# Optimization experiments

Hardware: AMD Instinct MI355X
Metric: run time of the kernel (lower is better)

The kernel has to match this reference:

```python
import jax, jax.numpy as jnp
import numpy as np

D_MODEL = 2048
NUM_HEADS = 16
HEAD_DIM = D_MODEL // NUM_HEADS
B, T = 4, 2048


def setup_inputs() -> dict:
    key = jax.random.key(0)
    ks = jax.random.split(key, 9)
    s = 1.0 / np.sqrt(D_MODEL)
    inp = {"x": jax.random.normal(ks[0], (B, T, D_MODEL), dtype=jnp.float32)}
    for i, name in enumerate(["q", "k", "v", "o"]):
        inp[f"W{name}"] = jax.random.uniform(ks[1 + 2 * i], (D_MODEL, D_MODEL), minval=-s, maxval=s, dtype=jnp.float32)
        inp[f"b{name}"] = jax.random.uniform(ks[2 + 2 * i], (D_MODEL,), minval=-s, maxval=s, dtype=jnp.float32)
    return inp


def reference(x, Wq, bq, Wk, bk, Wv, bv, Wo, bo):
    Bx, Tx, _ = x.shape
    H, Dh = NUM_HEADS, HEAD_DIM
    # torch Linear: y = x @ W.T + b
    q = (x @ Wq.T + bq).reshape(Bx, Tx, H, Dh).transpose(0, 2, 1, 3)  # [B,H,T,D]
    k = (x @ Wk.T + bk).reshape(Bx, Tx, H, Dh).transpose(0, 2, 1, 3)
    v = (x @ Wv.T + bv).reshape(Bx, Tx, H, Dh).transpose(0, 2, 1, 3)
    scale = 1.0 / np.sqrt(Dh).astype(np.float32)
    scores = jnp.einsum('bhqd,bhkd->bhqk', q, k) * scale  # [B,H,T,T] (no causal mask, as in source)
    attn = jax.nn.softmax(scores, axis=-1)
    out = jnp.einsum('bhqk,bhkd->bhqd', attn, v)  # [B,H,T,D]
    out = out.transpose(0, 2, 1, 3).reshape(Bx, Tx, H * Dh)
    return out @ Wo.T + bo
```

## Files before the change

### kernel.cpp

```cpp
#include <hip/hip_runtime.h>
#include <hip/hip_bf16.h>

typedef __bf16 bf16x8 __attribute__((ext_vector_type(8)));
typedef __bf16 bf16x4 __attribute__((ext_vector_type(4)));
typedef float floatx4 __attribute__((ext_vector_type(4)));

#define MFMA16(a, b, c) __builtin_amdgcn_mfma_f32_16x16x32_bf16((a), (b), (c), 0, 0, 0)

#define GLOAD16(g, l) __builtin_amdgcn_global_load_lds( \
    (const __attribute__((address_space(1))) unsigned int*)(g), \
    (__attribute__((address_space(3))) unsigned int*)(l), 16, 0, 0)

static constexpr int DM = 2048, NH = 16, HD = 128, BATCH = 4, SEQ = 2048;
static constexpr int MROWS = BATCH * SEQ;
static constexpr float SCALE = 0.08838834764831845f;
static constexpr float PMAX = 3.0f;

__global__ __launch_bounds__(256) void detect_dtype(
    const unsigned short* __restrict__ x, const unsigned short* __restrict__ w,
    int* __restrict__ flags) {
  const unsigned short* src = blockIdx.x ? w : x;
  const int tid = threadIdx.x;
  int cnt = 0;
  for (int i = tid; i < 4096; i += 256) {
    unsigned short u = src[2 * i];
    int e = (u >> 7) & 0xFF;
    cnt += (e >= 96 && e <= 158) ? 1 : 0;
  }
  __shared__ int s[256];
  s[tid] = cnt;
  __syncthreads();
  for (int off = 128; off > 0; off >>= 1) {
    if (tid < off) s[tid] += s[tid + off];
    __syncthreads();
  }
  if (tid == 0) flags[blockIdx.x] = (s[0] > 2560) ? 1 : 0;
}

__global__ __launch_bounds__(256) void cvt_f32_bf16(
    const float* __restrict__ src, __bf16* __restrict__ dst, int n,
    const int* __restrict__ flags) {
  if (flags[0] != 0) return;
  int stride = gridDim.x * 256 * 8;
  for (int i = (blockIdx.x * 256 + threadIdx.x) * 8; i < n; i += stride) {
    float4 a = *reinterpret_cast<const float4*>(src + i);
    float4 b = *reinterpret_cast<const float4*>(src + i + 4);
    bf16x8 r;
    r[0] = (__bf16)a.x; r[1] = (__bf16)a.y; r[2] = (__bf16)a.z; r[3] = (__bf16)a.w;
    r[4] = (__bf16)b.x; r[5] = (__bf16)b.y; r[6] = (__bf16)b.z; r[7] = (__bf16)b.w;
    *reinterpret_cast<bf16x8*>(dst + i) = r;
  }
}

__device__ __forceinline__ void gemm128_core(
    const __bf16* __restrict__ A, const __bf16* __restrict__ W,
    unsigned short* sA, unsigned short* sW,
    int tm, int tn, floatx4 (&acc)[4][4]) {
  const int tid = threadIdx.x;
  const int wave = tid >> 6, lane = tid & 63;
  const int q = lane >> 4, ml = lane & 15;
  const int waveM = (wave >> 1) * 64, waveN = (wave & 1) * 64;
  const int lrow = lane >> 3, cdst = lane & 7;
  const int csrc = cdst ^ (lrow & 7);

  for (int k0 = 0; k0 < DM; k0 += 64) {
    __syncthreads();
#pragma unroll
    for (int i = 0; i < 4; ++i) {
      int r0 = wave * 32 + i * 8;
      GLOAD16(A + (size_t)(tm + r0 + lrow) * DM + k0 + csrc * 8, &sA[r0 * 64]);
      GLOAD16(W + (size_t)(tn + r0 + lrow) * DM + k0 + csrc * 8, &sW[r0 * 64]);
    }
    __syncthreads();
#pragma unroll
    for (int s = 0; s < 2; ++s) {
      bf16x8 aF[4], bF[4];
#pragma unroll
      for (int t = 0; t < 4; ++t)
        aF[t] = *reinterpret_cast<const bf16x8*>(
            &sA[(waveM + t * 16 + ml) * 64 + (((s * 4 + q) ^ (ml & 7)) * 8)]);
#pragma unroll
      for (int t = 0; t < 4; ++t)
        bF[t] = *reinterpret_cast<const bf16x8*>(
            &sW[(waveN + t * 16 + ml) * 64 + (((s * 4 + q) ^ (ml & 7)) * 8)]);
#pragma unroll
      for (int rt = 0; rt < 4; ++rt)
#pragma unroll
        for (int ct = 0; ct < 4; ++ct)
          acc[rt][ct] = MFMA16(aF[rt], bF[ct], acc[rt][ct]);
    }
  }
}

__global__ __launch_bounds__(256) void qkv_gemm(
    const __bf16* __restrict__ X,
    const __bf16* __restrict__ Wq, const __bf16* __restrict__ Wk,
    const __bf16* __restrict__ Wv,
    const void* bq, const void* bk, const void* bv, int bias_f32,
    __bf16* __restrict__ qw, __bf16* __restrict__ kw, __bf16* __restrict__ vt,
    const int* __restrict__ flags, int wantX) {
  if (flags[0] != wantX) return;
  __shared__ unsigned short sA[128 * 64];
  __shared__ unsigned short sW[128 * 64];
  const int which = blockIdx.x >> 4;
  const int tn = (blockIdx.x & 15) * 128;
  const int tm = blockIdx.y * 128;
  const __bf16* W = which == 0 ? Wq : (which == 1 ? Wk : Wv);
  const void* bias = which == 0 ? bq : (which == 1 ? bk : bv);

  floatx4 acc[4][4] = {};
  gemm128_core(X, W, sA, sW, tm, tn, acc);

  const int tid = threadIdx.x, wave = tid >> 6, lane = tid & 63;
  const int q = lane >> 4, ml = lane & 15;
  const int waveM = (wave >> 1) * 64, waveN = (wave & 1) * 64;
#pragma unroll
  for (int ct = 0; ct < 4; ++ct) {
    int n = tn + waveN + ct * 16 + ml;
    float bv_ = bias_f32 ? ((const float*)bias)[n] : (float)((const __bf16*)bias)[n];
#pragma unroll
    for (int rt = 0; rt < 4; ++rt) {
      int m0 = tm + waveM + rt * 16 + q * 4;
      if (which < 2) {
        __bf16* dst = which == 0 ? qw : kw;
#pragma unroll
        for (int r = 0; r < 4; ++r)
          dst[(size_t)(m0 + r) * DM + n] = (__bf16)(acc[rt][ct][r] + bv_);
      } else {
        int h = n >> 7, d = n & 127, b = m0 >> 11, t = m0 & 2047;
        bf16x4 pk;
#pragma unroll
        for (int r = 0; r < 4; ++r) pk[r] = (__bf16)(acc[rt][ct][r] + bv_);
        *reinterpret_cast<bf16x4*>(vt + (size_t)((b * 16 + h) * 128 + d) * SEQ + t) = pk;
      }
    }
  }
}

__global__ __launch_bounds__(256) void proj_gemm(
    const __bf16* __restrict__ A, const __bf16* __restrict__ W,
    const void* bias, int bias_f32, void* out, int out_f32,
    const int* __restrict__ flags, int want) {
  if (flags[1] != want) return;
  __shared__ unsigned short sA[128 * 64];
  __shared__ unsigned short sW[128 * 64];
  const int tn = blockIdx.x * 128;
  const int tm = blockIdx.y * 128;

  floatx4 acc[4][4] = {};
  gemm128_core(A, W, sA, sW, tm, tn, acc);

  const int tid = threadIdx.x, wave = tid >> 6, lane = tid & 63;
  const int q = lane >> 4, ml = lane & 15;
  const int waveM = (wave >> 1) * 64, waveN = (wave & 1) * 64;
#pragma unroll
  for (int ct = 0; ct < 4; ++ct) {
    int n = tn + waveN + ct * 16 + ml;
    float bv_ = bias_f32 ? ((const float*)bias)[n] : (float)((const __bf16*)bias)[n];
#pragma unroll
    for (int rt = 0; rt < 4; ++rt) {
      int m0 = tm + waveM + rt * 16 + q * 4;
      if (out_f32) {
#pragma unroll
        for (int r = 0; r < 4; ++r)
          ((float*)out)[(size_t)(m0 + r) * DM + n] = acc[rt][ct][r] + bv_;
      } else {
#pragma unroll
        for (int r = 0; r < 4; ++r)
          ((__bf16*)out)[(size_t)(m0 + r) * DM + n] = (__bf16)(acc[rt][ct][r] + bv_);
      }
    }
  }
}

__device__ inline bf16x8 ld8s(const __bf16* p) {
  int4 v = *reinterpret_cast<const int4*>(p);
  return __builtin_bit_cast(bf16x8, v);
}
__device__ inline bf16x8 ld8s(const float* p) {
  float4 a = *reinterpret_cast<const float4*>(p);
  float4 b = *reinterpret_cast<const float4*>(p + 4);
  bf16x8 r;
  r[0] = (__bf16)a.x; r[1] = (__bf16)a.y; r[2] = (__bf16)a.z; r[3] = (__bf16)a.w;
  r[4] = (__bf16)b.x; r[5] = (__bf16)b.y; r[6] = (__bf16)b.z; r[7] = (__bf16)b.w;
  return r;
}

template <typename TA, typename TW>
__global__ __launch_bounds__(256) void gemm_slow(
    const TA* __restrict__ A, const TW* __restrict__ W,
    const TW* __restrict__ bias, void* __restrict__ C,
    int mode, int out_f32, const int* __restrict__ flags, int wantA, int wantW) {
  if (wantA >= 0 && flags[0] != wantA) return;
  if (wantW >= 0 && flags[1] != wantW) return;
  __shared__ unsigned short sA[128 * 72];
  __shared__ unsigned short sW[128 * 72];
  const int tid = threadIdx.x;
  const int tn = blockIdx.x * 128, tm = blockIdx.y * 128;
  const int wave = tid >> 6, lane = tid & 63;
  const int q = lane >> 4, ml = lane & 15;
  const int waveM = (wave >> 1) * 64, waveN = (wave & 1) * 64;
  const int srow = tid >> 3, sc8 = tid & 7;
  const int K = DM, N = DM;
  floatx4 acc[4][4] = {};
  for (int k0 = 0; k0 < K; k0 += 64) {
    bf16x8 va[4], vb[4];
#pragma unroll
    for (int i = 0; i < 4; ++i) {
      int row = srow + 32 * i;
      va[i] = ld8s(A + (size_t)(tm + row) * K + k0 + sc8 * 8);
      vb[i] = ld8s(W + (size_t)(tn + row) * K + k0 + sc8 * 8);
    }
    __syncthreads();
#pragma unroll
    for (int i = 0; i < 4; ++i) {
      int row = srow + 32 * i;
      *reinterpret_cast<int4*>(&sA[row * 72 + sc8 * 8]) = __builtin_bit_cast(int4, va[i]);
      *reinterpret_cast<int4*>(&sW[row * 72 + sc8 * 8]) = __builtin_bit_cast(int4, vb[i]);
    }
    __syncthreads();
#pragma unroll
    for (int s = 0; s < 2; ++s) {
      bf16x8 aF[4], bF[4];
#pragma unroll
      for (int t = 0; t < 4; ++t)
        aF[t] = *reinterpret_cast<const bf16x8*>(&sA[(waveM + t * 16 + ml) * 72 + s * 32 + q * 8]);
#pragma unroll
      for (int t = 0; t < 4; ++t)
        bF[t] = *reinterpret_cast<const bf16x8*>(&sW[(waveN + t * 16 + ml) * 72 + s * 32 + q * 8]);
#pragma unroll
      for (int rt = 0; rt < 4; ++rt)
#pragma unroll
        for (int ct = 0; ct < 4; ++ct)
          acc[rt][ct] = MFMA16(aF[rt], bF[ct], acc[rt][ct]);
    }
  }
#pragma unroll
  for (int ct = 0; ct < 4; ++ct) {
    int n = tn + waveN + ct * 16 + ml;
    float bv = (float)bias[n];
#pragma unroll
    for (int rt = 0; rt < 4; ++rt) {
      int mrow0 = tm + waveM + rt * 16 + q * 4;
      if (mode == 0) {
        if (out_f32) {
#pragma unroll
          for (int r = 0; r < 4; ++r)
            ((float*)C)[(size_t)(mrow0 + r) * N + n] = acc[rt][ct][r] + bv;
        } else {
#pragma unroll
          for (int r = 0; r < 4; ++r)
            ((__bf16*)C)[(size_t)(mrow0 + r) * N + n] = (__bf16)(acc[rt][ct][r] + bv);
        }
      } else {
        int h = n >> 7, d = n & 127, b = mrow0 >> 11, t = mrow0 & 2047;
        bf16x4 pk;
#pragma unroll
        for (int r = 0; r < 4; ++r) pk[r] = (__bf16)(acc[rt][ct][r] + bv);
        *reinterpret_cast<bf16x4*>((__bf16*)C + (size_t)((b * 16 + h) * 128 + d) * SEQ + t) = pk;
      }
    }
  }
}

__global__ __launch_bounds__(512) void mha_attn(
    const __bf16* __restrict__ Q, const __bf16* __restrict__ Kg,
    const __bf16* __restrict__ Vt, __bf16* __restrict__ O) {
  __shared__ unsigned short sK[64 * 128];
  __shared__ unsigned short sV[128 * 64];
  __shared__ unsigned short sP[128 * 72];

  const int tid = threadIdx.x;
  const int bh = blockIdx.y, b = bh >> 4, h = bh & 15;
  const int t0 = blockIdx.x * 128;
  const int wave = tid >> 6, lane = tid & 63;
  const int q = lane >> 4, ml = lane & 15;
  const int wrow = wave * 16;

  bf16x8 qf[4];
  {
    const __bf16* qrow = Q + (size_t)(b * SEQ + t0 + wrow + ml) * DM + h * HD;
#pragma unroll
    for (int s = 0; s < 4; ++s)
      qf[s] = *reinterpret_cast<const bf16x8*>(qrow + s * 32 + q * 8);
  }

  floatx4 oacc[8] = {};
  float lsum[4] = {0.f, 0.f, 0.f, 0.f};

  const __bf16* kbase = Kg + (size_t)(b * SEQ) * DM + h * HD;
  const __bf16* vbase = Vt + (size_t)bh * HD * SEQ;
  const int lrow4 = lane >> 4, c16 = lane & 15;
  const int lrow8 = lane >> 3, c8 = lane & 7;

  for (int kt = 0; kt < SEQ / 64; ++kt) {
    const int key0 = kt * 64;
    __syncthreads();
#pragma unroll
    for (int i = 0; i < 2; ++i) {
      int kr0 = wave * 8 + i * 4;
      int kc = c16 ^ ((i * 4 + lrow4) & 7);
      GLOAD16(kbase + (size_t)(key0 + kr0 + lrow4) * DM + kc * 8, &sK[kr0 * 128]);
      int vr0 = wave * 16 + i * 8;
      int vc = c8 ^ (lrow8 & 7);
      GLOAD16(vbase + (size_t)(vr0 + lrow8) * SEQ + key0 + vc * 8, &sV[vr0 * 64]);
    }
    __syncthreads();

    floatx4 sacc[4] = {};
#pragma unroll
    for (int s = 0; s < 4; ++s) {
#pragma unroll
      for (int ct = 0; ct < 4; ++ct) {
        bf16x8 kf = *reinterpret_cast<const bf16x8*>(
            &sK[(ct * 16 + ml) * 128 + (((s * 4 + q) ^ (ml & 7)) * 8)]);
        sacc[ct] = MFMA16(qf[s], kf, sacc[ct]);
      }
    }

#pragma unroll
    for (int ct = 0; ct < 4; ++ct) {
#pragma unroll
      for (int r = 0; r < 4; ++r) {
        float p = __expf(fmaf(sacc[ct][r], SCALE, -PMAX));
        sacc[ct][r] = p;
        lsum[r] += p;
        __bf16 pb = (__bf16)p;
        sP[(wrow + q * 4 + r) * 72 + ct * 16 + ml] = __builtin_bit_cast(unsigned short, pb);
      }
    }

#pragma unroll
    for (int s = 0; s < 2; ++s) {
      bf16x8 pf = *reinterpret_cast<const bf16x8*>(&sP[(wrow + ml) * 72 + s * 32 + q * 8]);
#pragma unroll
      for (int ot = 0; ot < 8; ++ot) {
        bf16x8 vf = *reinterpret_cast<const bf16x8*>(
            &sV[(ot * 16 + ml) * 64 + (((s * 4 + q) ^ (ml & 7)) * 8)]);
        oacc[ot] = MFMA16(pf, vf, oacc[ot]);
      }
    }
  }

#pragma unroll
  for (int r = 0; r < 4; ++r) {
    float s = lsum[r];
    s += __shfl_xor(s, 1); s += __shfl_xor(s, 2);
    s += __shfl_xor(s, 4); s += __shfl_xor(s, 8);
    lsum[r] = 1.0f / s;
  }
  __bf16* obase = O + (size_t)(b * SEQ + t0 + wrow) * DM + h * HD;
#pragma unroll
  for (int ot = 0; ot < 8; ++ot) {
    int d = ot * 16 + ml;
#pragma unroll
    for (int r = 0; r < 4; ++r)
      obase[(size_t)(q * 4 + r) * DM + d] = (__bf16)(oacc[ot][r] * lsum[r]);
  }
}

extern "C" void kernel_launch(void* const* d_in, const int* in_sizes, int n_in,
                              void* d_out, int out_size, void* d_ws, size_t ws_size,
                              hipStream_t stream) {
  const void* x  = d_in[0];
  const void* Wq = d_in[1]; const void* bq = d_in[2];
  const void* Wk = d_in[3]; const void* bk = d_in[4];
  const void* Wv = d_in[5]; const void* bv = d_in[6];
  const void* Wo = d_in[7]; const void* bo = d_in[8];

  int* flags = (int*)d_ws;
  const size_t XE = (size_t)MROWS * DM;
  const size_t WE = (size_t)DM * DM;

  detect_dtype<<<2, 256, 0, stream>>>((const unsigned short*)x, (const unsigned short*)Wq, flags);

  const size_t needA = 64 + 2 * XE * 2 + 4 * 2 * WE + 3 * 2 * XE;
  dim3 gq(48, 64), gp(16, 64), ga(SEQ / 128, BATCH * NH);

  if (ws_size >= needA + 256) {
    __bf16* xc  = (__bf16*)((char*)d_ws + 64);
    __bf16* Wqc = xc + XE;
    __bf16* Wkc = Wqc + WE;
    __bf16* Wvc = Wkc + WE;
    __bf16* Woc = Wvc + WE;
    __bf16* qw  = Woc + WE;
    __bf16* kw  = qw + XE;
    __bf16* vt  = kw + XE;
    __bf16* aw  = xc;

    cvt_f32_bf16<<<2048, 256, 0, stream>>>((const float*)x, xc, (int)XE, flags);
    cvt_f32_bf16<<<512, 256, 0, stream>>>((const float*)Wq, Wqc, (int)WE, flags);
    cvt_f32_bf16<<<512, 256, 0, stream>>>((const float*)Wk, Wkc, (int)WE, flags);
    cvt_f32_bf16<<<512, 256, 0, stream>>>((const float*)Wv, Wvc, (int)WE, flags);
    cvt_f32_bf16<<<512, 256, 0, stream>>>((const float*)Wo, Woc, (int)WE, flags);

    qkv_gemm<<<gq, 256, 0, stream>>>(xc, Wqc, Wkc, Wvc, bq, bk, bv, 1,
                                     qw, kw, vt, flags, 0);
    qkv_gemm<<<gq, 256, 0, stream>>>((const __bf16*)x, (const __bf16*)Wq,
                                     (const __bf16*)Wk, (const __bf16*)Wv,
                                     bq, bk, bv, 0, qw, kw, vt, flags, 1);
    mha_attn<<<ga, 512, 0, stream>>>(qw, kw, vt, aw);
    proj_gemm<<<gp, 256, 0, stream>>>(aw, Woc, bo, 1, d_out, 1, flags, 0);
    proj_gemm<<<gp, 256, 0, stream>>>(aw, (const __bf16*)Wo, bo, 0, d_out, 0, flags, 1);
  } else {
    __bf16* qw = (__bf16*)((char*)d_ws + 64);
    __bf16* kw = qw + XE;
    __bf16* vt = kw + XE;
    __bf16* aw = vt + XE;

    gemm_slow<float, float><<<gp, 256, 0, stream>>>(
        (const float*)x, (const float*)Wq, (const float*)bq, qw, 0, 0, flags, 0, 0);
    gemm_slow<float, float><<<gp, 256, 0, stream>>>(
        (const float*)x, (const float*)Wk, (const float*)bk, kw, 0, 0, flags, 0, 0);
    gemm_slow<float, float><<<gp, 256, 0, stream>>>(
        (const float*)x, (const float*)Wv, (const float*)bv, vt, 1, 0, flags, 0, 0);
    qkv_gemm<<<gq, 256, 0, stream>>>((const __bf16*)x, (const __bf16*)Wq,
                                     (const __bf16*)Wk, (const __bf16*)Wv,
                                     bq, bk, bv, 0, qw, kw, vt, flags, 1);
    mha_attn<<<ga, 512, 0, stream>>>(qw, kw, vt, aw);
    gemm_slow<__bf16, float><<<gp, 256, 0, stream>>>(
        aw, (const float*)Wo, (const float*)bo, d_out, 0, 1, flags, -1, 0);
    proj_gemm<<<gp, 256, 0, stream>>>(aw, (const __bf16*)Wo, bo, 0, d_out, 0, flags, 1);
  }
}
```

Baseline: 752.0 us.

## Drop dtype detection, fuse conversions, store Q/K head-major, reorder attention grid

Removes the runtime dtype-detection kernel and the duplicate bf16-path launches and assumes fp32 inputs. The five conversion kernels become one fused kernel over x and all weights. Q and K are now written in a per-head [B,H,T,D] layout, so attention loads them contiguously instead of with a 2048-element row stride. The attention grid is swapped so blocks sharing a head are adjacent, which may improve K/V cache reuse. This gives up support for bf16 inputs and adds scattered stores in the QKV epilogue.

```diff
diff --git a/kernel.cpp b/kernel.cpp
--- a/kernel.cpp
+++ b/kernel.cpp
@@ -16,35 +16,27 @@
 static constexpr float SCALE = 0.08838834764831845f;
 static constexpr float PMAX = 3.0f;
 
-__global__ __launch_bounds__(256) void detect_dtype(
-    const unsigned short* __restrict__ x, const unsigned short* __restrict__ w,
-    int* __restrict__ flags) {
-  const unsigned short* src = blockIdx.x ? w : x;
-  const int tid = threadIdx.x;
-  int cnt = 0;
-  for (int i = tid; i < 4096; i += 256) {
-    unsigned short u = src[2 * i];
-    int e = (u >> 7) & 0xFF;
-    cnt += (e >= 96 && e <= 158) ? 1 : 0;
-  }
-  __shared__ int s[256];
-  s[tid] = cnt;
-  __syncthreads();
-  for (int off = 128; off > 0; off >>= 1) {
-    if (tid < off) s[tid] += s[tid + off];
-    __syncthreads();
-  }
-  if (tid == 0) flags[blockIdx.x] = (s[0] > 2560) ? 1 : 0;
-}
-
-__global__ __launch_bounds__(256) void cvt_f32_bf16(
-    const float* __restrict__ src, __bf16* __restrict__ dst, int n,
-    const int* __restrict__ flags) {
-  if (flags[0] != 0) return;
-  int stride = gridDim.x * 256 * 8;
-  for (int i = (blockIdx.x * 256 + threadIdx.x) * 8; i < n; i += stride) {
-    float4 a = *reinterpret_cast<const float4*>(src + i);
-    float4 b = *reinterpret_cast<const float4*>(src + i + 4);
+static constexpr size_t XE = (size_t)MROWS * DM;
+static constexpr size_t WE = (size_t)DM * DM;
+
+__global__ __launch_bounds__(256) void cvt_all(
+    const float* __restrict__ x, const float* __restrict__ Wq,
+    const float* __restrict__ Wk, const float* __restrict__ Wv,
+    const float* __restrict__ Wo, __bf16* __restrict__ dst) {
+  const size_t total = XE + 4 * WE;
+  size_t stride = (size_t)gridDim.x * 256 * 8;
+  for (size_t i = ((size_t)blockIdx.x * 256 + threadIdx.x) * 8; i < total; i += stride) {
+    const float* src;
+    size_t off;
+    if (i < XE) { src = x; off = i; }
+    else {
+      size_t j = i - XE;
+      int seg = (int)(j / WE);
+      off = j - (size_t)seg * WE;
+      src = seg == 0 ? Wq : (seg == 1 ? Wk : (seg == 2 ? Wv : Wo));
+    }
+    float4 a = *reinterpret_cast<const float4*>(src + off);
+    float4 b = *reinterpret_cast<const float4*>(src + off + 4);
     bf16x8 r;
     r[0] = (__bf16)a.x; r[1] = (__bf16)a.y; r[2] = (__bf16)a.z; r[3] = (__bf16)a.w;
     r[4] = (__bf16)b.x; r[5] = (__bf16)b.y; r[6] = (__bf16)b.z; r[7] = (__bf16)b.w;
@@ -96,17 +88,16 @@
     const __bf16* __restrict__ X,
     const __bf16* __restrict__ Wq, const __bf16* __restrict__ Wk,
     const __bf16* __restrict__ Wv,
-    const void* bq, const void* bk, const void* bv, int bias_f32,
-    __bf16* __restrict__ qw, __bf16* __restrict__ kw, __bf16* __restrict__ vt,
-    const int* __restrict__ flags, int wantX) {
-  if (flags[0] != wantX) return;
+    const float* __restrict__ bq, const float* __restrict__ bk,
+    const float* __restrict__ bv,
+    __bf16* __restrict__ qh, __bf16* __restrict__ kh, __bf16* __restrict__ vt) {
   __shared__ unsigned short sA[128 * 64];
   __shared__ unsigned short sW[128 * 64];
   const int which = blockIdx.x >> 4;
   const int tn = (blockIdx.x & 15) * 128;
   const int tm = blockIdx.y * 128;
   const __bf16* W = which == 0 ? Wq : (which == 1 ? Wk : Wv);
-  const void* bias = which == 0 ? bq : (which == 1 ? bk : bv);
+  const float* bias = which == 0 ? bq : (which == 1 ? bk : bv);
 
   floatx4 acc[4][4] = {};
   gemm128_core(X, W, sA, sW, tm, tn, acc);
@@ -117,17 +108,18 @@
 #pragma unroll
   for (int ct = 0; ct < 4; ++ct) {
     int n = tn + waveN + ct * 16 + ml;
-    float bv_ = bias_f32 ? ((const float*)bias)[n] : (float)((const __bf16*)bias)[n];
+    float bv_ = bias[n];
+    int h = n >> 7, d = n & 127;
 #pragma unroll
     for (int rt = 0; rt < 4; ++rt) {
       int m0 = tm + waveM + rt * 16 + q * 4;
+      int b = m0 >> 11, t = m0 & 2047;
       if (which < 2) {
-        __bf16* dst = which == 0 ? qw : kw;
+        __bf16* dst = which == 0 ? qh : kh;
 #pragma unroll
         for (int r = 0; r < 4; ++r)
-          dst[(size_t)(m0 + r) * DM + n] = (__bf16)(acc[rt][ct][r] + bv_);
+          dst[((size_t)(b * 16 + h) * SEQ + t + r) * HD + d] = (__bf16)(acc[rt][ct][r] + bv_);
       } else {
-        int h = n >> 7, d = n & 127, b = m0 >> 11, t = m0 & 2047;
         bf16x4 pk;
 #pragma unroll
         for (int r = 0; r < 4; ++r) pk[r] = (__bf16)(acc[rt][ct][r] + bv_);
@@ -139,9 +131,7 @@
 
 __global__ __launch_bounds__(256) void proj_gemm(
     const __bf16* __restrict__ A, const __bf16* __restrict__ W,
-    const void* bias, int bias_f32, void* out, int out_f32,
-    const int* __restrict__ flags, int want) {
-  if (flags[1] != want) return;
+    const float* __restrict__ bias, float* __restrict__ out) {
   __shared__ unsigned short sA[128 * 64];
   __shared__ unsigned short sW[128 * 64];
   const int tn = blockIdx.x * 128;
@@ -156,27 +146,114 @@
 #pragma unroll
   for (int ct = 0; ct < 4; ++ct) {
     int n = tn + waveN + ct * 16 + ml;
-    float bv_ = bias_f32 ? ((const float*)bias)[n] : (float)((const __bf16*)bias)[n];
+    float bv_ = bias[n];
 #pragma unroll
     for (int rt = 0; rt < 4; ++rt) {
       int m0 = tm + waveM + rt * 16 + q * 4;
-      if (out_f32) {
-#pragma unroll
-        for (int r = 0; r < 4; ++r)
-          ((float*)out)[(size_t)(m0 + r) * DM + n] = acc[rt][ct][r] + bv_;
-      } else {
-#pragma unroll
-        for (int r = 0; r < 4; ++r)
-          ((__bf16*)out)[(size_t)(m0 + r) * DM + n] = (__bf16)(acc[rt][ct][r] + bv_);
-      }
-    }
-  }
-}
-
-__device__ inline bf16x8 ld8s(const __bf16* p) {
-  int4 v = *reinterpret_cast<const int4*>(p);
-  return __builtin_bit_cast(bf16x8, v);
-}
+#pragma unroll
+      for (int r = 0; r < 4; ++r)
+        out[(size_t)(m0 + r) * DM + n] = acc[rt][ct][r] + bv_;
+    }
+  }
+}
+
+__global__ __launch_bounds__(512) void mha_attn(
+    const __bf16* __restrict__ Q, const __bf16* __restrict__ Kg,
+    const __bf16* __restrict__ Vt, __bf16* __restrict__ O) {
+  __shared__ unsigned short sK[64 * 128];
+  __shared__ unsigned short sV[128 * 64];
+  __shared__ unsigned short sP[128 * 72];
+
+  const int tid = threadIdx.x;
+  const int bh = blockIdx.x;
+  const int t0 = blockIdx.y * 128;
+  const int wave = tid >> 6, lane = tid & 63;
+  const int q = lane >> 4, ml = lane & 15;
+  const int wrow = wave * 16;
+
+  bf16x8 qf[4];
+  {
+    const __bf16* qrow = Q + ((size_t)bh * SEQ + t0 + wrow + ml) * HD;
+#pragma unroll
+    for (int s = 0; s < 4; ++s)
+      qf[s] = *reinterpret_cast<const bf16x8*>(qrow + s * 32 + q * 8);
+  }
+
+  floatx4 oacc[8] = {};
+  float lsum[4] = {0.f, 0.f, 0.f, 0.f};
+
+  const __bf16* kbase = Kg + (size_t)bh * SEQ * HD;
+  const __bf16* vbase = Vt + (size_t)bh * HD * SEQ;
+  const int lrow4 = lane >> 4, c16 = lane & 15;
+  const int lrow8 = lane >> 3, c8 = lane & 7;
+
+  for (int kt = 0; kt < SEQ / 64; ++kt) {
+    const int key0 = kt * 64;
+    __syncthreads();
+#pragma unroll
+    for (int i = 0; i < 2; ++i) {
+      int kr0 = wave * 8 + i * 4;
+      int kc = c16 ^ ((i * 4 + lrow4) & 7);
+      GLOAD16(kbase + (size_t)(key0 + kr0 + lrow4) * HD + kc * 8, &sK[kr0 * 128]);
+      int vr0 = wave * 16 + i * 8;
+      int vc = c8 ^ (lrow8 & 7);
+      GLOAD16(vbase + (size_t)(vr0 + lrow8) * SEQ + key0 + vc * 8, &sV[vr0 * 64]);
+    }
+    __syncthreads();
+
+    floatx4 sacc[4] = {};
+#pragma unroll
+    for (int s = 0; s < 4; ++s) {
+#pragma unroll
+      for (int ct = 0; ct < 4; ++ct) {
+        bf16x8 kf = *reinterpret_cast<const bf16x8*>(
+            &sK[(ct * 16 + ml) * 128 + (((s * 4 + q) ^ (ml & 7)) * 8)]);
+        sacc[ct] = MFMA16(qf[s], kf, sacc[ct]);
+      }
+    }
+
+#pragma unroll
+    for (int ct = 0; ct < 4; ++ct) {
+#pragma unroll
+      for (int r = 0; r < 4; ++r) {
+        float p = __expf(fmaf(sacc[ct][r], SCALE, -PMAX));
+        sacc[ct][r] = p;
+        lsum[r] += p;
+        __bf16 pb = (__bf16)p;
+        sP[(wrow + q * 4 + r) * 72 + ct * 16 + ml] = __builtin_bit_cast(unsigned short, pb);
+      }
+    }
+
+#pragma unroll
+    for (int s = 0; s < 2; ++s) {
+      bf16x8 pf = *reinterpret_cast<const bf16x8*>(&sP[(wrow + ml) * 72 + s * 32 + q * 8]);
+#pragma unroll
+      for (int ot = 0; ot < 8; ++ot) {
+        bf16x8 vf = *reinterpret_cast<const bf16x8*>(
+            &sV[(ot * 16 + ml) * 64 + (((s * 4 + q) ^ (ml & 7)) * 8)]);
+        oacc[ot] = MFMA16(pf, vf, oacc[ot]);
+      }
+    }
+  }
+
+#pragma unroll
+  for (int r = 0; r < 4; ++r) {
+    float s = lsum[r];
+    s += __shfl_xor(s, 1); s += __shfl_xor(s, 2);
+    s += __shfl_xor(s, 4); s += __shfl_xor(s, 8);
+    lsum[r] = 1.0f / s;
+  }
+  const int b = bh >> 4, h = bh & 15;
+  __bf16* obase = O + ((size_t)b * SEQ + t0 + wrow) * DM + h * HD;
+#pragma unroll
+  for (int ot = 0; ot < 8; ++ot) {
+    int d = ot * 16 + ml;
+#pragma unroll
+    for (int r = 0; r < 4; ++r)
+      obase[(size_t)(q * 4 + r) * DM + d] = (__bf16)(oacc[ot][r] * lsum[r]);
+  }
+}
+
 __device__ inline bf16x8 ld8s(const float* p) {
   float4 a = *reinterpret_cast<const float4*>(p);
   float4 b = *reinterpret_cast<const float4*>(p + 4);
@@ -185,14 +262,15 @@
   r[4] = (__bf16)b.x; r[5] = (__bf16)b.y; r[6] = (__bf16)b.z; r[7] = (__bf16)b.w;
   return r;
 }
-
-template <typename TA, typename TW>
+__device__ inline bf16x8 ld8s(const __bf16* p) {
+  int4 v = *reinterpret_cast<const int4*>(p);
+  return __builtin_bit_cast(bf16x8, v);
+}
+
+template <typename TA>
 __global__ __launch_bounds__(256) void gemm_slow(
-    const TA* __restrict__ A, const TW* __restrict__ W,
-    const TW* __restrict__ bias, void* __restrict__ C,
-    int mode, int out_f32, const int* __restrict__ flags, int wantA, int wantW) {
-  if (wantA >= 0 && flags[0] != wantA) return;
-  if (wantW >= 0 && flags[1] != wantW) return;
+    const TA* __restrict__ A, const float* __restrict__ W,
+    const float* __restrict__ bias, void* __restrict__ C, int mode, int out_f32) {
   __shared__ unsigned short sA[128 * 72];
   __shared__ unsigned short sW[128 * 72];
   const int tid = threadIdx.x;
@@ -201,15 +279,14 @@
   const int q = lane >> 4, ml = lane & 15;
   const int waveM = (wave >> 1) * 64, waveN = (wave & 1) * 64;
   const int srow = tid >> 3, sc8 = tid & 7;
-  const int K = DM, N = DM;
   floatx4 acc[4][4] = {};
-  for (int k0 = 0; k0 < K; k0 += 64) {
+  for (int k0 = 0; k0 < DM; k0 += 64) {
     bf16x8 va[4], vb[4];
 #pragma unroll
     for (int i = 0; i < 4; ++i) {
       int row = srow + 32 * i;
-      va[i] = ld8s(A + (size_t)(tm + row) * K + k0 + sc8 * 8);
-      vb[i] = ld8s(W + (size_t)(tn + row) * K + k0 + sc8 * 8);
+      va[i] = ld8s(A + (size_t)(tm + row) * DM + k0 + sc8 * 8);
+      vb[i] = ld8s(W + (size_t)(tn + row) * DM + k0 + sc8 * 8);
     }
     __syncthreads();
 #pragma unroll
@@ -238,144 +315,48 @@
 #pragma unroll
   for (int ct = 0; ct < 4; ++ct) {
     int n = tn + waveN + ct * 16 + ml;
-    float bv = (float)bias[n];
+    float bv = bias[n];
+    int h = n >> 7, d = n & 127;
 #pragma unroll
     for (int rt = 0; rt < 4; ++rt) {
-      int mrow0 = tm + waveM + rt * 16 + q * 4;
+      int m0 = tm + waveM + rt * 16 + q * 4;
+      int b = m0 >> 11, t = m0 & 2047;
       if (mode == 0) {
         if (out_f32) {
 #pragma unroll
           for (int r = 0; r < 4; ++r)
-            ((float*)C)[(size_t)(mrow0 + r) * N + n] = acc[rt][ct][r] + bv;
+            ((float*)C)[(size_t)(m0 + r) * DM + n] = acc[rt][ct][r] + bv;
         } else {
 #pragma unroll
           for (int r = 0; r < 4; ++r)
-            ((__bf16*)C)[(size_t)(mrow0 + r) * N + n] = (__bf16)(acc[rt][ct][r] + bv);
+            ((__bf16*)C)[(size_t)(m0 + r) * DM + n] = (__bf16)(acc[rt][ct][r] + bv);
         }
-      } else {
-        int h = n >> 7, d = n & 127, b = mrow0 >> 11, t = mrow0 & 2047;
+      } else if (mode == 1) {
         bf16x4 pk;
 #pragma unroll
         for (int r = 0; r < 4; ++r) pk[r] = (__bf16)(acc[rt][ct][r] + bv);
         *reinterpret_cast<bf16x4*>((__bf16*)C + (size_t)((b * 16 + h) * 128 + d) * SEQ + t) = pk;
-      }
-    }
-  }
-}
-
-__global__ __launch_bounds__(512) void mha_attn(
-    const __bf16* __restrict__ Q, const __bf16* __restrict__ Kg,
-    const __bf16* __restrict__ Vt, __bf16* __restrict__ O) {
-  __shared__ unsigned short sK[64 * 128];
-  __shared__ unsigned short sV[128 * 64];
-  __shared__ unsigned short sP[128 * 72];
-
-  const int tid = threadIdx.x;
-  const int bh = blockIdx.y, b = bh >> 4, h = bh & 15;
-  const int t0 = blockIdx.x * 128;
-  const int wave = tid >> 6, lane = tid & 63;
-  const int q = lane >> 4, ml = lane & 15;
-  const int wrow = wave * 16;
-
-  bf16x8 qf[4];
-  {
-    const __bf16* qrow = Q + (size_t)(b * SEQ + t0 + wrow + ml) * DM + h * HD;
-#pragma unroll
-    for (int s = 0; s < 4; ++s)
-      qf[s] = *reinterpret_cast<const bf16x8*>(qrow + s * 32 + q * 8);
-  }
-
-  floatx4 oacc[8] = {};
-  float lsum[4] = {0.f, 0.f, 0.f, 0.f};
-
-  const __bf16* kbase = Kg + (size_t)(b * SEQ) * DM + h * HD;
-  const __bf16* vbase = Vt + (size_t)bh * HD * SEQ;
-  const int lrow4 = lane >> 4, c16 = lane & 15;
-  const int lrow8 = lane >> 3, c8 = lane & 7;
-
-  for (int kt = 0; kt < SEQ / 64; ++kt) {
-    const int key0 = kt * 64;
-    __syncthreads();
-#pragma unroll
-    for (int i = 0; i < 2; ++i) {
-      int kr0 = wave * 8 + i * 4;
-      int kc = c16 ^ ((i * 4 + lrow4) & 7);
-      GLOAD16(kbase + (size_t)(key0 + kr0 + lrow4) * DM + kc * 8, &sK[kr0 * 128]);
-      int vr0 = wave * 16 + i * 8;
-      int vc = c8 ^ (lrow8 & 7);
-      GLOAD16(vbase + (size_t)(vr0 + lrow8) * SEQ + key0 + vc * 8, &sV[vr0 * 64]);
-    }
-    __syncthreads();
-
-    floatx4 sacc[4] = {};
-#pragma unroll
-    for (int s = 0; s < 4; ++s) {
-#pragma unroll
-      for (int ct = 0; ct < 4; ++ct) {
-        bf16x8 kf = *reinterpret_cast<const bf16x8*>(
-            &sK[(ct * 16 + ml) * 128 + (((s * 4 + q) ^ (ml & 7)) * 8)]);
-        sacc[ct] = MFMA16(qf[s], kf, sacc[ct]);
-      }
-    }
-
-#pragma unroll
-    for (int ct = 0; ct < 4; ++ct) {
-#pragma unroll
-      for (int r = 0; r < 4; ++r) {
-        float p = __expf(fmaf(sacc[ct][r], SCALE, -PMAX));
-        sacc[ct][r] = p;
-        lsum[r] += p;
-        __bf16 pb = (__bf16)p;
-        sP[(wrow + q * 4 + r) * 72 + ct * 16 + ml] = __builtin_bit_cast(unsigned short, pb);
-      }
-    }
-
-#pragma unroll
-    for (int s = 0; s < 2; ++s) {
-      bf16x8 pf = *reinterpret_cast<const bf16x8*>(&sP[(wrow + ml) * 72 + s * 32 + q * 8]);
-#pragma unroll
-      for (int ot = 0; ot < 8; ++ot) {
-        bf16x8 vf = *reinterpret_cast<const bf16x8*>(
-            &sV[(ot * 16 + ml) * 64 + (((s * 4 + q) ^ (ml & 7)) * 8)]);
-        oacc[ot] = MFMA16(pf, vf, oacc[ot]);
-      }
-    }
-  }
-
-#pragma unroll
-  for (int r = 0; r < 4; ++r) {
-    float s = lsum[r];
-    s += __shfl_xor(s, 1); s += __shfl_xor(s, 2);
-    s += __shfl_xor(s, 4); s += __shfl_xor(s, 8);
-    lsum[r] = 1.0f / s;
-  }
-  __bf16* obase = O + (size_t)(b * SEQ + t0 + wrow) * DM + h * HD;
-#pragma unroll
-  for (int ot = 0; ot < 8; ++ot) {
-    int d = ot * 16 + ml;
-#pragma unroll
-    for (int r = 0; r < 4; ++r)
-      obase[(size_t)(q * 4 + r) * DM + d] = (__bf16)(oacc[ot][r] * lsum[r]);
+      } else {
+#pragma unroll
+        for (int r = 0; r < 4; ++r)
+          ((__bf16*)C)[((size_t)(b * 16 + h) * SEQ + t + r) * HD + d] =
+              (__bf16)(acc[rt][ct][r] + bv);
+      }
+    }
   }
 }
 
 extern "C" void kernel_launch(void* const* d_in, const int* in_sizes, int n_in,
                               void* d_out, int out_size, void* d_ws, size_t ws_size,
                               hipStream_t stream) {
-  const void* x  = d_in[0];
-  const void* Wq = d_in[1]; const void* bq = d_in[2];
-  const void* Wk = d_in[3]; const void* bk = d_in[4];
-  const void* Wv = d_in[5]; const void* bv = d_in[6];
-  const void* Wo = d_in[7]; const void* bo = d_in[8];
-
-  int* flags = (int*)d_ws;
-  const size_t XE = (size_t)MROWS * DM;
-  const size_t WE = (size_t)DM * DM;
-
-  detect_dtype<<<2, 256, 0, stream>>>((const unsigned short*)x, (const unsigned short*)Wq, flags);
-
-  const size_t needA = 64 + 2 * XE * 2 + 4 * 2 * WE + 3 * 2 * XE;
-  dim3 gq(48, 64), gp(16, 64), ga(SEQ / 128, BATCH * NH);
+  const float* x  = (const float*)d_in[0];
+  const float* Wq = (const float*)d_in[1]; const float* bq = (const float*)d_in[2];
+  const float* Wk = (const float*)d_in[3]; const float* bk = (const float*)d_in[4];
+  const float* Wv = (const float*)d_in[5]; const float* bv = (const float*)d_in[6];
+  const float* Wo = (const float*)d_in[7]; const float* bo = (const float*)d_in[8];
+
+  const size_t needA = 64 + 2 * (4 * XE + 4 * WE);
+  dim3 gq(48, 64), gp(16, 64), ga(BATCH * NH, SEQ / 128);
 
   if (ws_size >= needA + 256) {
     __bf16* xc  = (__bf16*)((char*)d_ws + 64);
@@ -383,43 +364,24 @@
     __bf16* Wkc = Wqc + WE;
     __bf16* Wvc = Wkc + WE;
     __bf16* Woc = Wvc + WE;
-    __bf16* qw  = Woc + WE;
-    __bf16* kw  = qw + XE;
-    __bf16* vt  = kw + XE;
+    __bf16* qh  = Woc + WE;
+    __bf16* kh  = qh + XE;
+    __bf16* vt  = kh + XE;
     __bf16* aw  = xc;
 
-    cvt_f32_bf16<<<2048, 256, 0, stream>>>((const float*)x, xc, (int)XE, flags);
-    cvt_f32_bf16<<<512, 256, 0, stream>>>((const float*)Wq, Wqc, (int)WE, flags);
-    cvt_f32_bf16<<<512, 256, 0, stream>>>((const float*)Wk, Wkc, (int)WE, flags);
-    cvt_f32_bf16<<<512, 256, 0, stream>>>((const float*)Wv, Wvc, (int)WE, flags);
-    cvt_f32_bf16<<<512, 256, 0, stream>>>((const float*)Wo, Woc, (int)WE, flags);
-
-    qkv_gemm<<<gq, 256, 0, stream>>>(xc, Wqc, Wkc, Wvc, bq, bk, bv, 1,
-                                     qw, kw, vt, flags, 0);
-    qkv_gemm<<<gq, 256, 0, stream>>>((const __bf16*)x, (const __bf16*)Wq,
-                                     (const __bf16*)Wk, (const __bf16*)Wv,
-                                     bq, bk, bv, 0, qw, kw, vt, flags, 1);
-    mha_attn<<<ga, 512, 0, stream>>>(qw, kw, vt, aw);
-    proj_gemm<<<gp, 256, 0, stream>>>(aw, Woc, bo, 1, d_out, 1, flags, 0);
-    proj_gemm<<<gp, 256, 0, stream>>>(aw, (const __bf16*)Wo, bo, 0, d_out, 0, flags, 1);
+    cvt_all<<<4096, 256, 0, stream>>>(x, Wq, Wk, Wv, Wo, xc);
+    qkv_gemm<<<gq, 256, 0, stream>>>(xc, Wqc, Wkc, Wvc, bq, bk, bv, qh, kh, vt);
+    mha_attn<<<ga, 512, 0, stream>>>(qh, kh, vt, aw);
+    proj_gemm<<<gp, 256, 0, stream>>>(aw, Woc, bo, (float*)d_out);
   } else {
-    __bf16* qw = (__bf16*)((char*)d_ws + 64);
-    __bf16* kw = qw + XE;
-    __bf16* vt = kw + XE;
+    __bf16* qh = (__bf16*)((char*)d_ws + 64);
+    __bf16* kh = qh + XE;
+    __bf16* vt = kh + XE;
     __bf16* aw = vt + XE;
-
-    gemm_slow<float, float><<<gp, 256, 0, stream>>>(
-        (const float*)x, (const float*)Wq, (const float*)bq, qw, 0, 0, flags, 0, 0);
-    gemm_slow<float, float><<<gp, 256, 0, stream>>>(
-        (const float*)x, (const float*)Wk, (const float*)bk, kw, 0, 0, flags, 0, 0);
-    gemm_slow<float, float><<<gp, 256, 0, stream>>>(
-        (const float*)x, (const float*)Wv, (const float*)bv, vt, 1, 0, flags, 0, 0);
-    qkv_gemm<<<gq, 256, 0, stream>>>((const __bf16*)x, (const __bf16*)Wq,
-                                     (const __bf16*)Wk, (const __bf16*)Wv,
-                                     bq, bk, bv, 0, qw, kw, vt, flags, 1);
-    mha_attn<<<ga, 512, 0, stream>>>(qw, kw, vt, aw);
-    gemm_slow<__bf16, float><<<gp, 256, 0, stream>>>(
-        aw, (const float*)Wo, (const float*)bo, d_out, 0, 1, flags, -1, 0);
-    proj_gemm<<<gp, 256, 0, stream>>>(aw, (const __bf16*)Wo, bo, 0, d_out, 0, flags, 1);
-  }
-}
+    gemm_slow<float><<<gp, 256, 0, stream>>>(x, Wq, bq, qh, 2, 0);
+    gemm_slow<float><<<gp, 256, 0, stream>>>(x, Wk, bk, kh, 2, 0);
+    gemm_slow<float><<<gp, 256, 0, stream>>>(x, Wv, bv, vt, 1, 0);
+    mha_attn<<<ga, 512, 0, stream>>>(qh, kh, vt, aw);
+    gemm_slow<__bf16><<<gp, 256, 0, stream>>>(aw, Wo, bo, d_out, 0, 1);
+  }
+}
```

New measurement: 727.2 us. 1.03x faster.
